# Optimization experiments

Hardware: AMD Instinct MI355X
Metric: run time of the kernel (lower is better)

The kernel has to match this reference:

```python
import jax, jax.numpy as jnp
import numpy as np

B, N, NS, D = 32, 1024, 8, 768
HID = max(D, 128)  # hidden_dim = max(dim, hidden_dim)
ITERS = 3
EPS = 1e-8        # slot-attention renorm eps
LN_EPS = 1e-5     # torch LayerNorm default
SCALE = D ** -0.5


def _layernorm(x, g, b):
    m = jnp.mean(x, axis=-1, keepdims=True)
    v = jnp.mean((x - m) ** 2, axis=-1, keepdims=True)
    return (x - m) * jax.lax.rsqrt(v + LN_EPS) * g + b


def setup_inputs() -> dict:
    key = jax.random.key(0)
    ks = jax.random.split(key, 12)

    def lin_w(k, fan_in, fan_out):
        # xavier-uniform-like init; stored as [in, out] for x @ W
        lim = np.sqrt(6.0 / (fan_in + fan_out)).astype(np.float32)
        return jax.random.uniform(k, (fan_in, fan_out), jnp.float32, -lim, lim)

    return {
        "slots": jax.random.normal(ks[0], (1, NS, D), jnp.float32),
        "inputs": jax.random.normal(ks[1], (B, N, D), jnp.float32),
        "Wq": lin_w(ks[2], D, D), "bq": jnp.zeros((D,), jnp.float32),
        "Wk": lin_w(ks[3], D, D), "bk": jnp.zeros((D,), jnp.float32),
        "Wv": lin_w(ks[4], D, D), "bv": jnp.zeros((D,), jnp.float32),
        "g_in": jnp.ones((D,), jnp.float32), "b_in": jnp.zeros((D,), jnp.float32),
        "g_s": jnp.ones((D,), jnp.float32), "b_s": jnp.zeros((D,), jnp.float32),
        "g_ff": jnp.ones((D,), jnp.float32), "b_ff": jnp.zeros((D,), jnp.float32),
        "W1": lin_w(ks[5], D, HID), "b1": jnp.zeros((HID,), jnp.float32),
        "W2": lin_w(ks[6], HID, D), "b2": jnp.zeros((D,), jnp.float32),
    }


def reference(slots, inputs, Wq, bq, Wk, bk, Wv, bv,
              g_in, b_in, g_s, b_s, g_ff, b_ff, W1, b1, W2, b2):
    b = inputs.shape[0]
    slots = jnp.broadcast_to(slots, (b,) + slots.shape[1:])  # [b, ns, d]

    x = _layernorm(inputs, g_in, b_in)
    k = x @ Wk + bk  # [b, n, d]
    v = x @ Wv + bv  # [b, n, d]

    attn = None
    for _ in range(ITERS):
        slots_prev = slots
        sn = _layernorm(slots, g_s, b_s)
        q = sn @ Wq + bq                                  # [b, ns, d]
        dots = jnp.einsum('bid,bjd->bij', q, k) * SCALE   # [b, ns, n]
        attn = jax.nn.softmax(dots, axis=1)               # softmax over slots
        attn = attn / (jnp.sum(attn, axis=-1, keepdims=True) + EPS)
        updates = jnp.einsum('bjd,bij->bid', v, attn)     # [b, ns, d]
        h = _layernorm(updates, g_ff, b_ff)
        slots = slots_prev + jax.nn.relu(h @ W1 + b1) @ W2 + b2 * 0 + (jax.nn.relu(h @ W1 + b1) @ W2 + b2 - (jax.nn.relu(h @ W1 + b1) @ W2)) * 0
        slots = slots_prev + (jax.nn.relu(h @ W1 + b1) @ W2 + b2)

    return slots, jnp.transpose(attn, (0, 2, 1))  # ([b,ns,d], [b,n,ns])
```

## Files before the change

### kernel.cpp

```cpp
#include <hip/hip_runtime.h>

#define LNEPS 1e-5f
#define AEPS 1e-8f
#define SCALE_Q 0.036084391824351615f

typedef unsigned int uint32;

__device__ inline uint32 bfb(float f) {
  __bf16 h = (__bf16)f;
  unsigned short u;
  __builtin_memcpy(&u, &h, 2);
  return (uint32)u;
}

__global__ void setup_k(const float* __restrict__ Wk, float* __restrict__ WkT,
                        const float* __restrict__ s0, float* __restrict__ slots) {
  __shared__ float tile[32][33];
  int bb = blockIdx.x, t = threadIdx.x;
  if (bb < 576) {
    int c0 = (bb % 24) * 32, i0 = (bb / 24) * 32;
    int tx = t & 31, ty = t >> 5;
#pragma unroll
    for (int k = 0; k < 4; ++k)
      tile[ty + 8 * k][tx] = Wk[(size_t)(i0 + ty + 8 * k) * 768 + c0 + tx];
    __syncthreads();
#pragma unroll
    for (int k = 0; k < 4; ++k)
      WkT[(size_t)(c0 + ty + 8 * k) * 768 + i0 + tx] = tile[tx][ty + 8 * k];
  } else {
    int idx = (bb - 576) * 256 + t;
    slots[idx] = s0[idx % 6144];
  }
}

template <bool LN, int MODE>
__global__ void gemv_k(const float* __restrict__ X, const float* __restrict__ W,
                       const float* __restrict__ bias, const float* __restrict__ gamma,
                       const float* __restrict__ beta_ln, const float* __restrict__ alpha,
                       const float* __restrict__ beta, float* __restrict__ out) {
  __shared__ float XsT[768 * 12];
  int t = threadIdx.x;
  int c0 = blockIdx.x * 64, r0 = blockIdx.y * 8;
#pragma unroll
  for (int j = 0; j < 3; ++j) {
    int fidx = j * 512 + t;
    int r = fidx / 192, c4 = fidx % 192;
    float4 v = *(const float4*)(X + (size_t)(r0 + r) * 768 + c4 * 4);
    int kb = c4 * 4;
    XsT[(kb + 0) * 12 + r] = v.x;
    XsT[(kb + 1) * 12 + r] = v.y;
    XsT[(kb + 2) * 12 + r] = v.z;
    XsT[(kb + 3) * 12 + r] = v.w;
  }
  __syncthreads();
  if (LN) {
    int w = t >> 6, l = t & 63;
    float s = 0.f, ss = 0.f;
#pragma unroll
    for (int m = 0; m < 12; ++m) {
      float x = XsT[(l + 64 * m) * 12 + w];
      s += x; ss += x * x;
    }
#pragma unroll
    for (int o = 32; o; o >>= 1) { s += __shfl_xor(s, o); ss += __shfl_xor(ss, o); }
    float mu = s * (1.f / 768.f), rs = rsqrtf(ss * (1.f / 768.f) - mu * mu + LNEPS);
#pragma unroll
    for (int m = 0; m < 12; ++m) {
      int d = l + 64 * m;
      XsT[d * 12 + w] = (XsT[d * 12 + w] - mu) * rs * gamma[d] + beta_ln[d];
    }
    __syncthreads();
  }
  int cx = t & 63, kg = t >> 6;
  int c = c0 + cx;
  float acc[8] = {};
  const float* wp = W + c;
  int k0 = kg * 96;
#pragma unroll 8
  for (int k = k0; k < k0 + 96; ++k) {
    float wv = wp[(size_t)k * 768];
    float4 xa = *(const float4*)&XsT[k * 12];
    float4 xb = *(const float4*)&XsT[k * 12 + 4];
    acc[0] += xa.x * wv; acc[1] += xa.y * wv; acc[2] += xa.z * wv; acc[3] += xa.w * wv;
    acc[4] += xb.x * wv; acc[5] += xb.y * wv; acc[6] += xb.z * wv; acc[7] += xb.w * wv;
  }
  __syncthreads();
  float* red = XsT;
  if (kg > 0) {
#pragma unroll
    for (int r = 0; r < 8; ++r) red[((kg - 1) * 8 + r) * 64 + cx] = acc[r];
  }
  __syncthreads();
  if (kg == 0) {
#pragma unroll
    for (int g = 1; g < 8; ++g)
#pragma unroll
      for (int r = 0; r < 8; ++r) acc[r] += red[((g - 1) * 8 + r) * 64 + cx];
    float bsc = (MODE == 1) ? 0.f : bias[c];
#pragma unroll
    for (int r = 0; r < 8; ++r) {
      int rr = r0 + r;
      size_t oidx = (size_t)rr * 768 + c;
      float v;
      if (MODE == 0) v = acc[r] + bsc;
      else if (MODE == 1) v = acc[r];
      else if (MODE == 2) v = acc[r] * alpha[rr] + bsc * beta[rr];
      else if (MODE == 3) v = fmaxf(acc[r] + bsc, 0.f);
      else v = out[oidx] + acc[r] + bsc;
      out[oidx] = v;
    }
  }
}

__global__ void qprep_k(const float* __restrict__ q, const float* __restrict__ qk,
                        const float* __restrict__ g_in, const float* __restrict__ b_in,
                        const float* __restrict__ bk, float* __restrict__ Sqbuf,
                        float* __restrict__ c0buf) {
  int row = blockIdx.x * 4 + (threadIdx.x >> 6), l = threadIdx.x & 63;
  float aS = 0.f, aC = 0.f;
#pragma unroll
  for (int j = 0; j < 12; ++j) {
    int d = l + 64 * j;
    float qkv = qk[(size_t)row * 768 + d];
    aS += qkv * g_in[d];
    aC += qkv * b_in[d] + q[(size_t)row * 768 + d] * bk[d];
  }
#pragma unroll
  for (int o = 32; o; o >>= 1) { aS += __shfl_xor(aS, o); aC += __shfl_xor(aC, o); }
  if (l == 0) { Sqbuf[row] = aS; c0buf[row] = aC; }
}

template <bool FIRST>
__global__ void __launch_bounds__(512, 2)
dotspool_k(const float* __restrict__ inf, uint32* __restrict__ xh,
           const float* __restrict__ qk, const float* __restrict__ g_in,
           const float* __restrict__ Sqbuf, const float* __restrict__ c0buf,
           float* __restrict__ attnbuf, float* __restrict__ partials,
           float* __restrict__ A0p, float* __restrict__ A1p) {
  __shared__ float qkgs[8][768];
  __shared__ uint32 xt[32 * 390];
  __shared__ float oa[64][8], ow[64][8], orm[64];
  __shared__ float c0s[8], Sqs[8];
  int chunk = blockIdx.x, b = blockIdx.y, t = threadIdx.x, w = t >> 6, l = t & 63;
  for (int i = t; i < 6144; i += 512)
    ((float*)qkgs)[i] = qk[(size_t)b * 6144 + i] * g_in[i % 768];
  if (t < 8) { c0s[t] = c0buf[b * 8 + t]; Sqs[t] = Sqbuf[b * 8 + t]; }
  int g = l & 15, grp = l >> 4;
  float pacc[8][2] = {};
#pragma unroll
  for (int sub = 0; sub < 2; ++sub) {
    if (FIRST) {
      const float4* xpf =
          (const float4*)(inf + ((size_t)b * 1024 + chunk * 64 + sub * 32) * 768);
      uint2* xg = (uint2*)(xh + ((size_t)b * 1024 + chunk * 64 + sub * 32) * 384);
#pragma unroll
      for (int j = 0; j < 12; ++j) {
        int idx = j * 512 + t;
        int row = idx / 192, c4 = idx % 192;
        float4 v = xpf[(size_t)row * 192 + c4];
        uint2 o;
        o.x = bfb(v.x) | (bfb(v.y) << 16);
        o.y = bfb(v.z) | (bfb(v.w) << 16);
        xt[row * 390 + c4 * 2] = o.x;
        xt[row * 390 + c4 * 2 + 1] = o.y;
        xg[(size_t)row * 192 + c4] = o;
      }
    } else {
      const uint32* xps = xh + ((size_t)b * 1024 + chunk * 64) * 384 + sub * 12288;
#pragma unroll
      for (int j = 0; j < 24; ++j) {
        int idx = j * 512 + t;
        xt[(idx / 384) * 390 + (idx % 384)] = xps[idx];
      }
    }
    __syncthreads();
    {
      int lr32 = w * 4 + grp;
      int lr = sub * 32 + lr32;
      size_t row = (size_t)b * 1024 + chunk * 64 + lr;
      const uint32* xr = &xt[lr32 * 390];
      float s = 0.f, ss = 0.f, ds[8] = {};
#pragma unroll 8
      for (int j = 0; j < 24; ++j) {
        uint32 u = xr[j * 16 + g];
        float a = __uint_as_float(u << 16);
        float bv = __uint_as_float(u & 0xffff0000u);
        s += a + bv;
        ss += a * a + bv * bv;
        int d0 = 2 * (j * 16 + g);
#pragma unroll
        for (int s2 = 0; s2 < 8; ++s2) {
          float2 qg = *(const float2*)&qkgs[s2][d0];
          ds[s2] += qg.x * a + qg.y * bv;
        }
      }
#pragma unroll
      for (int o = 1; o < 16; o <<= 1) {
        s += __shfl_xor(s, o);
        ss += __shfl_xor(ss, o);
#pragma unroll
        for (int s2 = 0; s2 < 8; ++s2) ds[s2] += __shfl_xor(ds[s2], o);
      }
      float mu = s * (1.f / 768.f), r = rsqrtf(ss * (1.f / 768.f) - mu * mu + LNEPS);
      float rmu = r * mu;
      float sc[8];
#pragma unroll
      for (int s2 = 0; s2 < 8; ++s2)
        sc[s2] = (r * ds[s2] - rmu * Sqs[s2] + c0s[s2]) * SCALE_Q;
      float mx = sc[0];
#pragma unroll
      for (int s2 = 1; s2 < 8; ++s2) mx = fmaxf(mx, sc[s2]);
      float e[8], se = 0.f;
#pragma unroll
      for (int s2 = 0; s2 < 8; ++s2) { e[s2] = __expf(sc[s2] - mx); se += e[s2]; }
      float inv_se = 1.f / se;
      float av = e[0];
#pragma unroll
      for (int s2 = 1; s2 < 8; ++s2) av = (g == s2) ? e[s2] : av;
      av *= inv_se;
      if (g < 8) {
        oa[lr][g] = av;
        ow[lr][g] = av * r;
      }
      if (g == 8) orm[lr] = rmu;
      (void)row;
    }
    __syncthreads();
    if (t < 384) {
#pragma unroll 2
      for (int nn = 0; nn < 32; ++nn) {
        uint32 u = xt[nn * 390 + t];
        float x0 = __uint_as_float(u << 16);
        float x1 = __uint_as_float(u & 0xffff0000u);
#pragma unroll
        for (int s2 = 0; s2 < 8; ++s2) {
          float wv = ow[sub * 32 + nn][s2];
          pacc[s2][0] += wv * x0; pacc[s2][1] += wv * x1;
        }
      }
    } else if (sub == 1 && t < 392) {
      int sl = t - 384;
      float A0 = 0.f, A1 = 0.f;
      for (int rr2 = 0; rr2 < 64; ++rr2) {
        float a = oa[rr2][sl];
        A0 += a;
        A1 += a * orm[rr2];
      }
      A0p[chunk * 256 + b * 8 + sl] = A0;
      A1p[chunk * 256 + b * 8 + sl] = A1;
    }
    __syncthreads();
  }
  if (t < 384) {
#pragma unroll
    for (int s2 = 0; s2 < 8; ++s2) {
      size_t base = ((size_t)(chunk * 256 + b * 8 + s2)) * 768;
      float2 v; v.x = pacc[s2][0]; v.y = pacc[s2][1];
      *(float2*)&partials[base + 2 * t] = v;
    }
  }
  size_t base8 = ((size_t)b * 1024 + chunk * 64) * 8;
  attnbuf[base8 + t] = oa[t >> 3][t & 7];
}

__global__ void reduce_fix_k(const float* __restrict__ partials, const float* __restrict__ A0p,
                             const float* __restrict__ A1p, const float* __restrict__ g_in,
                             const float* __restrict__ b_in, float* __restrict__ pooled,
                             float* __restrict__ invbuf, float* __restrict__ rhobuf) {
  int row = blockIdx.x, t = threadIdx.x;
  float A0 = 0.f, A1 = 0.f;
#pragma unroll
  for (int ch = 0; ch < 16; ++ch) {
    A0 += A0p[ch * 256 + row];
    A1 += A1p[ch * 256 + row];
  }
#pragma unroll
  for (int c = 0; c < 3; ++c) {
    int d = t + 256 * c;
    float a = 0.f;
    for (int ch = 0; ch < 16; ++ch) a += partials[((size_t)(ch * 256 + row)) * 768 + d];
    pooled[(size_t)row * 768 + d] = g_in[d] * (a - A1) + b_in[d] * A0;
  }
  if (t == 0) {
    float iv = 1.f / (A0 + AEPS);
    invbuf[row] = iv;
    rhobuf[row] = A0 * iv;
  }
}

__global__ void outs_k(const float* __restrict__ slots, const float* __restrict__ attnbuf,
                       const float* __restrict__ invbuf, float* __restrict__ out) {
  int i = blockIdx.x * 256 + threadIdx.x;
  if (i < 196608) {
    out[i] = slots[i];
  } else {
    int j = i - 196608;
    out[i] = attnbuf[j] * invbuf[((j >> 13) << 3) + (j & 7)];
  }
}

extern "C" void kernel_launch(void* const* d_in, const int* in_sizes, int n_in,
                              void* d_out, int out_size, void* d_ws, size_t ws_size,
                              hipStream_t stream) {
  (void)in_sizes; (void)n_in; (void)out_size; (void)ws_size;
  const float* slots0 = (const float*)d_in[0];
  const float* inputs = (const float*)d_in[1];
  const float* Wq = (const float*)d_in[2];
  const float* bq = (const float*)d_in[3];
  const float* Wk = (const float*)d_in[4];
  const float* bk = (const float*)d_in[5];
  const float* Wv = (const float*)d_in[6];
  const float* bv = (const float*)d_in[7];
  const float* g_in = (const float*)d_in[8];
  const float* b_in = (const float*)d_in[9];
  const float* g_s = (const float*)d_in[10];
  const float* b_s = (const float*)d_in[11];
  const float* g_ff = (const float*)d_in[12];
  const float* b_ff = (const float*)d_in[13];
  const float* W1 = (const float*)d_in[14];
  const float* b1 = (const float*)d_in[15];
  const float* W2 = (const float*)d_in[16];
  const float* b2 = (const float*)d_in[17];

  char* p = (char*)d_ws;
  uint32* xh = (uint32*)p;     p += (size_t)32768 * 384 * 4;
  float* WkT = (float*)p;      p += (size_t)768 * 768 * 4;
  float* slotsf = (float*)p;   p += 256 * 768 * 4;
  float* qbuf = (float*)p;     p += 256 * 768 * 4;
  float* qkbuf = (float*)p;    p += 256 * 768 * 4;
  float* Sqbuf = (float*)p;    p += 256 * 4;
  float* c0buf = (float*)p;    p += 256 * 4;
  float* attnbuf = (float*)p;  p += (size_t)32768 * 8 * 4;
  float* partials = (float*)p; p += (size_t)16 * 256 * 768 * 4;
  float* A0p = (float*)p;      p += 16 * 256 * 4;
  float* A1p = (float*)p;      p += 16 * 256 * 4;
  float* pooled = (float*)p;   p += 256 * 768 * 4;
  float* invbuf = (float*)p;   p += 256 * 4;
  float* rhobuf = (float*)p;   p += 256 * 4;
  float* updbuf = (float*)p;   p += 256 * 768 * 4;
  float* t1buf = (float*)p;    p += 256 * 768 * 4;

  dim3 ggrid(12, 32);
  setup_k<<<1344, 256, 0, stream>>>(Wk, WkT, slots0, slotsf);
  for (int it = 0; it < 3; ++it) {
    gemv_k<true, 0><<<ggrid, 512, 0, stream>>>(slotsf, Wq, bq, g_s, b_s, nullptr, nullptr,
                                               qbuf);
    gemv_k<false, 1><<<ggrid, 512, 0, stream>>>(qbuf, WkT, nullptr, nullptr, nullptr, nullptr,
                                                nullptr, qkbuf);
    qprep_k<<<64, 256, 0, stream>>>(qbuf, qkbuf, g_in, b_in, bk, Sqbuf, c0buf);
    if (it == 0)
      dotspool_k<true><<<dim3(16, 32), 512, 0, stream>>>(inputs, xh, qkbuf, g_in, Sqbuf,
                                                         c0buf, attnbuf, partials, A0p, A1p);
    else
      dotspool_k<false><<<dim3(16, 32), 512, 0, stream>>>(inputs, xh, qkbuf, g_in, Sqbuf,
                                                          c0buf, attnbuf, partials, A0p, A1p);
    reduce_fix_k<<<256, 256, 0, stream>>>(partials, A0p, A1p, g_in, b_in, pooled,
                                          invbuf, rhobuf);
    gemv_k<false, 2><<<ggrid, 512, 0, stream>>>(pooled, Wv, bv, nullptr, nullptr, invbuf,
                                                rhobuf, updbuf);
    gemv_k<true, 3><<<ggrid, 512, 0, stream>>>(updbuf, W1, b1, g_ff, b_ff, nullptr, nullptr,
                                               t1buf);
    gemv_k<false, 4><<<ggrid, 512, 0, stream>>>(t1buf, W2, b2, nullptr, nullptr, nullptr,
                                                nullptr, slotsf);
  }
  outs_k<<<1792, 256, 0, stream>>>(slotsf, attnbuf, invbuf, (float*)d_out);
}
```

Measured before the change: 343.7 us.

## Vectorize dotspool with packed f32x2 math, wider LDS copies, 32-lane row groups

Rewrites the dotspool kernel's inner loops around f32x2 ext_vector types so the compiler can emit packed FP32 ops (v_pk_fma_f32) for the LN stats, the q·x dot products and the attention-weighted pooling. The LDS row stride is padded to 392 so tiles can be staged with uint2/uint4 stores, and global-to-LDS copies now use 16-byte loads. Each row is now reduced by 32 lanes instead of 16, with every wave handling two rows per pass, which adds one more shuffle stage. The aim is fewer issued ALU and memory instructions per element, at the cost of a changed bank-conflict pattern from the new stride.

```diff
diff --git a/kernel.cpp b/kernel.cpp
--- a/kernel.cpp
+++ b/kernel.cpp
@@ -5,6 +5,7 @@
 #define SCALE_Q 0.036084391824351615f
 
 typedef unsigned int uint32;
+typedef float f32x2 __attribute__((ext_vector_type(2)));
 
 __device__ inline uint32 bfb(float f) {
   __bf16 h = (__bf16)f;
@@ -138,15 +139,15 @@
            float* __restrict__ attnbuf, float* __restrict__ partials,
            float* __restrict__ A0p, float* __restrict__ A1p) {
   __shared__ float qkgs[8][768];
-  __shared__ uint32 xt[32 * 390];
+  __shared__ uint32 xt[32 * 392];
   __shared__ float oa[64][8], ow[64][8], orm[64];
   __shared__ float c0s[8], Sqs[8];
   int chunk = blockIdx.x, b = blockIdx.y, t = threadIdx.x, w = t >> 6, l = t & 63;
   for (int i = t; i < 6144; i += 512)
     ((float*)qkgs)[i] = qk[(size_t)b * 6144 + i] * g_in[i % 768];
   if (t < 8) { c0s[t] = c0buf[b * 8 + t]; Sqs[t] = Sqbuf[b * 8 + t]; }
-  int g = l & 15, grp = l >> 4;
-  float pacc[8][2] = {};
+  int g32 = l & 31, grp = l >> 5;
+  f32x2 pacc[8] = {};
 #pragma unroll
   for (int sub = 0; sub < 2; ++sub) {
     if (FIRST) {
@@ -161,41 +162,48 @@
         uint2 o;
         o.x = bfb(v.x) | (bfb(v.y) << 16);
         o.y = bfb(v.z) | (bfb(v.w) << 16);
-        xt[row * 390 + c4 * 2] = o.x;
-        xt[row * 390 + c4 * 2 + 1] = o.y;
+        *(uint2*)&xt[row * 392 + c4 * 2] = o;
         xg[(size_t)row * 192 + c4] = o;
       }
     } else {
-      const uint32* xps = xh + ((size_t)b * 1024 + chunk * 64) * 384 + sub * 12288;
-#pragma unroll
-      for (int j = 0; j < 24; ++j) {
+      const uint4* xps4 = (const uint4*)(xh + ((size_t)b * 1024 + chunk * 64) * 384 +
+                                         sub * 12288);
+#pragma unroll
+      for (int j = 0; j < 6; ++j) {
         int idx = j * 512 + t;
-        xt[(idx / 384) * 390 + (idx % 384)] = xps[idx];
-      }
-    }
-    __syncthreads();
-    {
-      int lr32 = w * 4 + grp;
+        int row = idx / 96, c4 = idx % 96;
+        *(uint4*)&xt[row * 392 + c4 * 4] = xps4[idx];
+      }
+    }
+    __syncthreads();
+#pragma unroll
+    for (int rr = 0; rr < 2; ++rr) {
+      int lr32 = rr * 16 + w * 2 + grp;
       int lr = sub * 32 + lr32;
-      size_t row = (size_t)b * 1024 + chunk * 64 + lr;
-      const uint32* xr = &xt[lr32 * 390];
-      float s = 0.f, ss = 0.f, ds[8] = {};
-#pragma unroll 8
-      for (int j = 0; j < 24; ++j) {
-        uint32 u = xr[j * 16 + g];
-        float a = __uint_as_float(u << 16);
-        float bv = __uint_as_float(u & 0xffff0000u);
-        s += a + bv;
-        ss += a * a + bv * bv;
-        int d0 = 2 * (j * 16 + g);
+      const uint32* xr = &xt[lr32 * 392];
+      f32x2 sv = {0.f, 0.f}, ssv = {0.f, 0.f};
+      f32x2 ds2[8] = {};
+#pragma unroll 4
+      for (int j = 0; j < 12; ++j) {
+        uint32 u = xr[j * 32 + g32];
+        f32x2 ab;
+        ab.x = __uint_as_float(u << 16);
+        ab.y = __uint_as_float(u & 0xffff0000u);
+        sv += ab;
+        ssv += ab * ab;
+        int d0 = 2 * (j * 32 + g32);
 #pragma unroll
         for (int s2 = 0; s2 < 8; ++s2) {
-          float2 qg = *(const float2*)&qkgs[s2][d0];
-          ds[s2] += qg.x * a + qg.y * bv;
+          f32x2 qg = *(const f32x2*)&qkgs[s2][d0];
+          ds2[s2] += qg * ab;
         }
       }
-#pragma unroll
-      for (int o = 1; o < 16; o <<= 1) {
+      float s = sv.x + sv.y, ss = ssv.x + ssv.y;
+      float ds[8];
+#pragma unroll
+      for (int s2 = 0; s2 < 8; ++s2) ds[s2] = ds2[s2].x + ds2[s2].y;
+#pragma unroll
+      for (int o = 1; o < 32; o <<= 1) {
         s += __shfl_xor(s, o);
         ss += __shfl_xor(ss, o);
 #pragma unroll
@@ -216,26 +224,28 @@
       float inv_se = 1.f / se;
       float av = e[0];
 #pragma unroll
-      for (int s2 = 1; s2 < 8; ++s2) av = (g == s2) ? e[s2] : av;
+      for (int s2 = 1; s2 < 8; ++s2) av = (g32 == s2) ? e[s2] : av;
       av *= inv_se;
-      if (g < 8) {
-        oa[lr][g] = av;
-        ow[lr][g] = av * r;
-      }
-      if (g == 8) orm[lr] = rmu;
-      (void)row;
+      if (g32 < 8) {
+        oa[lr][g32] = av;
+        ow[lr][g32] = av * r;
+      }
+      if (g32 == 8) orm[lr] = rmu;
     }
     __syncthreads();
     if (t < 384) {
 #pragma unroll 2
       for (int nn = 0; nn < 32; ++nn) {
-        uint32 u = xt[nn * 390 + t];
-        float x0 = __uint_as_float(u << 16);
-        float x1 = __uint_as_float(u & 0xffff0000u);
-#pragma unroll
-        for (int s2 = 0; s2 < 8; ++s2) {
-          float wv = ow[sub * 32 + nn][s2];
-          pacc[s2][0] += wv * x0; pacc[s2][1] += wv * x1;
+        uint32 u = xt[nn * 392 + t];
+        f32x2 xv;
+        xv.x = __uint_as_float(u << 16);
+        xv.y = __uint_as_float(u & 0xffff0000u);
+        const float* owr = &ow[sub * 32 + nn][0];
+#pragma unroll
+        for (int k = 0; k < 4; ++k) {
+          f32x2 owv = *(const f32x2*)&owr[2 * k];
+          pacc[2 * k] += owv.x * xv;
+          pacc[2 * k + 1] += owv.y * xv;
         }
       }
     } else if (sub == 1 && t < 392) {
@@ -255,8 +265,7 @@
 #pragma unroll
     for (int s2 = 0; s2 < 8; ++s2) {
       size_t base = ((size_t)(chunk * 256 + b * 8 + s2)) * 768;
-      float2 v; v.x = pacc[s2][0]; v.y = pacc[s2][1];
-      *(float2*)&partials[base + 2 * t] = v;
+      *(f32x2*)&partials[base + 2 * t] = pacc[s2];
     }
   }
   size_t base8 = ((size_t)b * 1024 + chunk * 64) * 8;
```

New measurement: 350.5 us. No clear change (+2.0%).
